# Kernel optimization log

Hardware: AMD Instinct MI355X
Metric: run time of the kernel (lower is better)

## Reference

```python
import jax, jax.numpy as jnp
import numpy as np
from jax import lax

# Config (matches init_kwargs)
B, CIN, H, W = 32, 256, 56, 56
COUT, KS, STRIDE, PAD, GROUPS = 256, 3, 1, 1, 2
CG_IN = CIN // GROUPS            # 128
OUT_F = COUT // GROUPS           # 128 per-group out features
IN_F = CG_IN * KS * KS           # 1152 per-group in features
Q = (IN_F * OUT_F // 4) * GROUPS # 73728 quadruplets total
TAU = 1.0

# All six 2-of-4 masking patterns (as in the torch module)
_MASK_PATTERNS = np.array([[0.,0.,1.,1.],[0.,1.,0.,1.],[0.,1.,1.,0.],
                           [1.,0.,0.,1.],[1.,0.,1.,0.],[1.,1.,0.,0.]], dtype=np.float32)


def setup_inputs() -> dict:
    key = jax.random.key(0)
    k1, k2, k3, k4 = jax.random.split(key, 4)
    x = jax.random.normal(k1, (B, CIN, H, W), dtype=jnp.float32)
    # per-group weight blocks, xavier-ish scale
    Ws = jax.random.normal(k2, (GROUPS, OUT_F, IN_F), dtype=jnp.float32) * 0.03
    choice_weights = jax.random.normal(k3, (Q, 6), dtype=jnp.float32)
    # gumbel noise: -log(Exp(1)) ~ Gumbel(0,1), matching -empty.exponential_().log()
    gumbels = -jnp.log(jax.random.exponential(k4, (Q, 6), dtype=jnp.float32))
    masking_patterns = jnp.asarray(_MASK_PATTERNS)
    return {"x": x, "Ws": Ws, "choice_weights": choice_weights,
            "gumbels": gumbels, "masking_patterns": masking_patterns}


def _hard_gumbel_softmax(logits, gumbels, tau):
    # straight-through hard gumbel softmax over last dim
    y_soft = jax.nn.softmax((logits + gumbels) / tau, axis=-1)
    idx = jnp.argmax(y_soft, axis=-1)
    y_hard = jax.nn.one_hot(idx, logits.shape[-1], dtype=logits.dtype)
    return y_hard - lax.stop_gradient(y_soft) + y_soft


def reference(x, Ws, choice_weights, gumbels, masking_patterns):
    # 1) sample 2:4 mask per quadruplet via hard gumbel-softmax choice over 6 patterns
    choice = _hard_gumbel_softmax(choice_weights, gumbels, TAU)   # (Q, 6)
    mask = choice @ masking_patterns                              # (Q, 4)
    mask = mask.reshape(GROUPS, OUT_F, IN_F)                      # quadruplets tile W row-major
    Wm = Ws * mask                                                # (G, OUT_F, IN_F)

    # 2) im2col (torch Unfold ordering: channel-major, then kh, kw)
    patches = lax.conv_general_dilated_patches(
        x, filter_shape=(KS, KS), window_strides=(STRIDE, STRIDE),
        padding=[(PAD, PAD), (PAD, PAD)])                         # (B, CIN*KS*KS, Ho, Wo)
    Ho = (H + 2 * PAD - KS) // STRIDE + 1
    Wo = (W + 2 * PAD - KS) // STRIDE + 1
    L = Ho * Wo
    # channel-major ordering => group g occupies contiguous IN_F rows
    patches = patches.reshape(B, GROUPS, IN_F, L)                 # (B, G, IN_F, L)

    # 3) per-group masked GEMM, no bias (use_bias=False)
    y = jnp.einsum('goi,bgil->bgol', Wm, patches)                 # (B, G, OUT_F, L)
    return y.reshape(B, COUT, Ho, Wo)
```

## Files before the change

### kernel.cpp

```cpp
#include <hip/hip_runtime.h>


#define INF   1152
#define HO    56
#define LOUT  3136
#define XP    58

typedef __attribute__((ext_vector_type(8))) short bf16x8;
typedef __attribute__((ext_vector_type(4))) float f32x4;

__device__ __forceinline__ unsigned short f2bf(float f) {
  union { float f; unsigned u; } v; v.f = f;
  unsigned r = v.u + 0x7fffu + ((v.u >> 16) & 1u);
  return (unsigned short)(r >> 16);
}

__device__ __forceinline__ void async_load16(const void* g, void* l) {
  __builtin_amdgcn_global_load_lds(
      (const __attribute__((address_space(1))) void*)g,
      (__attribute__((address_space(3))) void*)l, 16, 0, 0);
}

__global__ __launch_bounds__(256) void prep_kernel(
    const float* __restrict__ x, const float* __restrict__ Ws,
    const float* __restrict__ cw, const float* __restrict__ gb,
    const float* __restrict__ pat,
    unsigned short* __restrict__ Xt, unsigned short* __restrict__ Wt) {
  __shared__ float lds[56 * 129];
  const int t   = threadIdx.x;
  const int bid = blockIdx.x;

  if (bid >= 3712) {
    int idx = (bid - 3712) * 256 + t;
    int c   = idx & 127;
    int of  = (idx >> 7) & 127;
    int gt  = idx >> 14;
    int g   = gt / 9;
    int tap = gt - g * 9;
    int e   = ((g << 7) + of) * INF + c * 9 + tap;
    int q   = e >> 2, pos = e & 3;
    const float* cq = cw + q * 6;
    const float* gq = gb + q * 6;
    float best = cq[0] + gq[0]; int bi = 0;
    #pragma unroll
    for (int j = 1; j < 6; ++j) {
      float v2 = cq[j] + gq[j];
      if (v2 > best) { best = v2; bi = j; }
    }
    Wt[idx] = f2bf(Ws[e] * pat[bi * 4 + pos]);
    return;
  }

  const int bg  = bid / 58;
  const int ihp = bid - bg * 58;
  uint4* dst = (uint4*)(Xt + ((bg * XP + ihp) * XP) * 128);
  if (ihp == 0 || ihp == XP - 1) {
    const uint4 z = {0u, 0u, 0u, 0u};
    for (int i = t; i < XP * 16; i += 256) dst[i] = z;
    return;
  }
  const int ih = ihp - 1;
  const float4* src = (const float4*)(x + (bg * 128) * LOUT + ih * HO);
  for (int i = t; i < 128 * 14; i += 256) {
    int c = i / 14, seg = i - c * 14;
    float4 v = src[c * (LOUT / 4) + seg];
    float* row = &lds[(seg * 4) * 129 + c];
    row[0]       = v.x;
    row[129]     = v.y;
    row[2 * 129] = v.z;
    row[3 * 129] = v.w;
  }
  __syncthreads();
  for (int i = t; i < XP * 16; i += 256) {
    int iwp = i >> 4, oct = i & 15;
    uint4 val = {0u, 0u, 0u, 0u};
    if (iwp != 0 && iwp != XP - 1) {
      const float* s = &lds[(iwp - 1) * 129 + (oct << 3)];
      val.x = (unsigned)f2bf(s[0]) | ((unsigned)f2bf(s[1]) << 16);
      val.y = (unsigned)f2bf(s[2]) | ((unsigned)f2bf(s[3]) << 16);
      val.z = (unsigned)f2bf(s[4]) | ((unsigned)f2bf(s[5]) << 16);
      val.w = (unsigned)f2bf(s[6]) | ((unsigned)f2bf(s[7]) << 16);
    }
    dst[i] = val;
  }
}

__global__ __launch_bounds__(256, 4) void conv_mfma_kernel(
    const unsigned short* __restrict__ Wt, const unsigned short* __restrict__ Xt,
    float* __restrict__ out) {
  __shared__ __align__(16) unsigned short sA[128 * 64];
  __shared__ __align__(16) unsigned short sB[128 * 64];
  const int t  = threadIdx.x;
  const int ln = t & 63, wv = t >> 6;
  const int wm = wv >> 1, wn = wv & 1;
  const int col = ln & 15, kq = ln >> 4, c7 = col & 7;

  const int lid   = blockIdx.y * 25 + blockIdx.x;
  const int v     = (lid & 7) * 200 + (lid >> 3);
  const int bg    = v / 25;
  const int tileN = v - bg * 25;
  const int g     = bg & 1;
  const int l0    = tileN << 7;

  const int r8 = ln >> 3;
  const int ch = (ln & 7) ^ r8;
  int arow[4], brow[4];
  #pragma unroll
  for (int i = 0; i < 4; ++i) {
    const int rr = (wv << 5) + (i << 3) + r8;
    arow[i] = (rr << 7) + (ch << 3);
    int ll = l0 + rr;
    if (ll > LOUT - 1) ll = LOUT - 1;
    int oh = ll / HO, ow = ll - oh * HO;
    brow[i] = ((bg * XP + oh) * XP + ow) * 128 + (ch << 3);
  }

  f32x4 acc[4][4];
  #pragma unroll
  for (int i = 0; i < 4; ++i)
    #pragma unroll
    for (int j = 0; j < 4; ++j) acc[i][j] = (f32x4){0.f, 0.f, 0.f, 0.f};

  for (int tap = 0; tap < 9; ++tap) {
    const int th = tap / 3, tw = tap - th * 3;
    const int bTap = (th * XP + tw) << 7;
    const int aTap = (g * 9 + tap) << 14;
    #pragma unroll 1
    for (int kc = 0; kc < 2; ++kc) {
      const int c0 = kc << 6;
      __syncthreads();
      #pragma unroll
      for (int i = 0; i < 4; ++i) {
        const int lb = ((wv << 5) + (i << 3)) << 6;
        async_load16(Wt + aTap + c0 + arow[i], &sA[lb]);
        async_load16(Xt + bTap + c0 + brow[i], &sB[lb]);
      }
      __syncthreads();
      #pragma unroll
      for (int kh = 0; kh < 2; ++kh) {
        const int pk = (((kh << 2) + kq) ^ c7) << 3;
        bf16x8 af[4], bfr[4];
        #pragma unroll
        for (int mi = 0; mi < 4; ++mi)
          af[mi] = *(const bf16x8*)&sA[(((wm << 6) + (mi << 4) + col) << 6) + pk];
        #pragma unroll
        for (int ni = 0; ni < 4; ++ni)
          bfr[ni] = *(const bf16x8*)&sB[(((wn << 6) + (ni << 4) + col) << 6) + pk];
        #pragma unroll
        for (int mi = 0; mi < 4; ++mi)
          #pragma unroll
          for (int ni = 0; ni < 4; ++ni)
            acc[mi][ni] = __builtin_amdgcn_mfma_f32_16x16x32_bf16(
                af[mi], bfr[ni], acc[mi][ni], 0, 0, 0);
      }
    }
  }

  const int rowq = kq << 2;
  #pragma unroll
  for (int mi = 0; mi < 4; ++mi) {
    #pragma unroll
    for (int ni = 0; ni < 4; ++ni) {
      const int l = l0 + (wn << 6) + (ni << 4) + col;
      if (l < LOUT) {
        #pragma unroll
        for (int r = 0; r < 4; ++r) {
          const int of = (wm << 6) + (mi << 4) + rowq + r;
          out[(bg * 128 + of) * LOUT + l] = acc[mi][ni][r];
        }
      }
    }
  }
}

extern "C" void kernel_launch(void* const* d_in, const int* in_sizes, int n_in,
                              void* d_out, int out_size, void* d_ws, size_t ws_size,
                              hipStream_t stream) {
  const float* x   = (const float*)d_in[0];
  const float* Ws  = (const float*)d_in[1];
  const float* cw  = (const float*)d_in[2];
  const float* gb  = (const float*)d_in[3];
  const float* pat = (const float*)d_in[4];
  float* out = (float*)d_out;

  unsigned short* Wt = (unsigned short*)d_ws;
  unsigned short* Xt = (unsigned short*)((char*)d_ws + (1 << 20));

  prep_kernel<<<4864, 256, 0, stream>>>(x, Ws, cw, gb, pat, Xt, Wt);
  conv_mfma_kernel<<<dim3(25, 64), 256, 0, stream>>>(Wt, Xt, out);
}
```

Measured before the change: 254.4 us.

## Double-buffer LDS tiles to overlap async global loads with MFMA compute

Splits the A and B shared-memory tiles into two buffers and flattens the tap/channel-chunk loops into 18 stages. Each stage issues the async global-to-LDS loads for the next stage before running MFMAs on the current one, which removes one barrier per stage. LDS use doubles to 64 KB and the launch-bounds occupancy hint drops from 4 to 2 blocks per CU, so there may be fewer waves resident to hide latency.

```diff
diff --git a/kernel.cpp b/kernel.cpp
--- a/kernel.cpp
+++ b/kernel.cpp
@@ -85,11 +85,11 @@
   }
 }
 
-__global__ __launch_bounds__(256, 4) void conv_mfma_kernel(
+__global__ __launch_bounds__(256, 2) void conv_mfma_kernel(
     const unsigned short* __restrict__ Wt, const unsigned short* __restrict__ Xt,
     float* __restrict__ out) {
-  __shared__ __align__(16) unsigned short sA[128 * 64];
-  __shared__ __align__(16) unsigned short sB[128 * 64];
+  __shared__ __align__(16) unsigned short sA[2][128 * 64];
+  __shared__ __align__(16) unsigned short sB[2][128 * 64];
   const int t  = threadIdx.x;
   const int ln = t & 63, wv = t >> 6;
   const int wm = wv >> 1, wn = wv & 1;
@@ -121,39 +121,45 @@
     #pragma unroll
     for (int j = 0; j < 4; ++j) acc[i][j] = (f32x4){0.f, 0.f, 0.f, 0.f};
 
-  for (int tap = 0; tap < 9; ++tap) {
-    const int th = tap / 3, tw = tap - th * 3;
-    const int bTap = (th * XP + tw) << 7;
-    const int aTap = (g * 9 + tap) << 14;
-    #pragma unroll 1
-    for (int kc = 0; kc < 2; ++kc) {
-      const int c0 = kc << 6;
-      __syncthreads();
+  auto issue = [&](int s, int nxt) {
+    const int tap = s >> 1, kc = s & 1;
+    const int th  = (tap * 11) >> 5;
+    const int tw  = tap - th * 3;
+    const int bOff = ((th * XP + tw) << 7) + (kc << 6);
+    const int aOff = ((g * 9 + tap) << 14) + (kc << 6);
+    #pragma unroll
+    for (int i = 0; i < 4; ++i) {
+      const int lb = ((wv << 5) + (i << 3)) << 6;
+      async_load16(Wt + aOff + arow[i], &sA[nxt][lb]);
+      async_load16(Xt + bOff + brow[i], &sB[nxt][lb]);
+    }
+  };
+
+  issue(0, 0);
+  __syncthreads();
+
+  #pragma unroll 2
+  for (int s = 0; s < 18; ++s) {
+    const int cur = s & 1;
+    if (s < 17) issue(s + 1, cur ^ 1);
+    #pragma unroll
+    for (int kh = 0; kh < 2; ++kh) {
+      const int pk = (((kh << 2) + kq) ^ c7) << 3;
+      bf16x8 af[4], bfr[4];
       #pragma unroll
-      for (int i = 0; i < 4; ++i) {
-        const int lb = ((wv << 5) + (i << 3)) << 6;
-        async_load16(Wt + aTap + c0 + arow[i], &sA[lb]);
-        async_load16(Xt + bTap + c0 + brow[i], &sB[lb]);
-      }
-      __syncthreads();
+      for (int mi = 0; mi < 4; ++mi)
+        af[mi] = *(const bf16x8*)&sA[cur][(((wm << 6) + (mi << 4) + col) << 6) + pk];
       #pragma unroll
-      for (int kh = 0; kh < 2; ++kh) {
-        const int pk = (((kh << 2) + kq) ^ c7) << 3;
-        bf16x8 af[4], bfr[4];
-        #pragma unroll
-        for (int mi = 0; mi < 4; ++mi)
-          af[mi] = *(const bf16x8*)&sA[(((wm << 6) + (mi << 4) + col) << 6) + pk];
+      for (int ni = 0; ni < 4; ++ni)
+        bfr[ni] = *(const bf16x8*)&sB[cur][(((wn << 6) + (ni << 4) + col) << 6) + pk];
+      #pragma unroll
+      for (int mi = 0; mi < 4; ++mi)
         #pragma unroll
         for (int ni = 0; ni < 4; ++ni)
-          bfr[ni] = *(const bf16x8*)&sB[(((wn << 6) + (ni << 4) + col) << 6) + pk];
-        #pragma unroll
-        for (int mi = 0; mi < 4; ++mi)
-          #pragma unroll
-          for (int ni = 0; ni < 4; ++ni)
-            acc[mi][ni] = __builtin_amdgcn_mfma_f32_16x16x32_bf16(
-                af[mi], bfr[ni], acc[mi][ni], 0, 0, 0);
-      }
+          acc[mi][ni] = __builtin_amdgcn_mfma_f32_16x16x32_bf16(
+              af[mi], bfr[ni], acc[mi][ni], 0, 0, 0);
     }
+    __syncthreads();
   }
 
   const int rowq = kq << 2;
```

New measurement: 271.5 us. 6.7% more time.

## Stage input halo tile in LDS once per channel chunk and double-buffer weights

Applied to the files above, without the earlier changes.

Instead of reloading a fresh 128x64 im2col B tile for each of the 9 taps, each block loads a 6-row by 64-column padded input halo window (384 pixels x 64 channels) into LDS once per channel chunk. Each tap then reads its shifted window directly from that LDS tile, and the weight tile is double-buffered so the next tap's A load overlaps the current MFMAs. This cuts global/L2 traffic for the input by about 9x and removes one barrier per tap. In exchange LDS use rises to 80KB per block and the launch bound drops to 2 blocks per CU, lowering occupancy.

```diff
diff --git a/kernel.cpp b/kernel.cpp
--- a/kernel.cpp
+++ b/kernel.cpp
@@ -85,11 +85,11 @@
   }
 }
 
-__global__ __launch_bounds__(256, 4) void conv_mfma_kernel(
+__global__ __launch_bounds__(256, 2) void conv_mfma_kernel(
     const unsigned short* __restrict__ Wt, const unsigned short* __restrict__ Xt,
     float* __restrict__ out) {
-  __shared__ __align__(16) unsigned short sA[128 * 64];
-  __shared__ __align__(16) unsigned short sB[128 * 64];
+  __shared__ __align__(16) unsigned short sA[2][128 * 64];
+  __shared__ __align__(16) unsigned short sB[384 * 64];
   const int t  = threadIdx.x;
   const int ln = t & 63, wv = t >> 6;
   const int wm = wv >> 1, wn = wv & 1;
@@ -101,19 +101,32 @@
   const int tileN = v - bg * 25;
   const int g     = bg & 1;
   const int l0    = tileN << 7;
+  const int oh0   = l0 / HO;
 
   const int r8 = ln >> 3;
   const int ch = (ln & 7) ^ r8;
-  int arow[4], brow[4];
-  #pragma unroll
-  for (int i = 0; i < 4; ++i) {
-    const int rr = (wv << 5) + (i << 3) + r8;
-    arow[i] = (rr << 7) + (ch << 3);
-    int ll = l0 + rr;
-    if (ll > LOUT - 1) ll = LOUT - 1;
-    int oh = ll / HO, ow = ll - oh * HO;
-    brow[i] = ((bg * XP + oh) * XP + ow) * 128 + (ch << 3);
-  }
+  int arow[4];
+  #pragma unroll
+  for (int i = 0; i < 4; ++i)
+    arow[i] = (((wv << 5) + (i << 3) + r8) << 7) + (ch << 3);
+
+  const int p0    = t >> 3;
+  const int kB    = (t & 7) ^ (p0 & 7);
+  const int xbase = bg * (XP * XP * 128);
+
+  int pb[4];
+  #pragma unroll
+  for (int ni = 0; ni < 4; ++ni) {
+    int l = l0 + (wn << 6) + (ni << 4) + col;
+    if (l > LOUT - 1) l = LOUT - 1;
+    int oh = l / HO, ow = l - oh * HO;
+    pb[ni] = ((oh - oh0) << 6) + ow;
+  }
+
+  int aoffm[4];
+  #pragma unroll
+  for (int mi = 0; mi < 4; ++mi)
+    aoffm[mi] = (((wm << 6) + (mi << 4) + col) << 6) + ((kq ^ c7) << 3);
 
   f32x4 acc[4][4];
   #pragma unroll
@@ -121,31 +134,49 @@
     #pragma unroll
     for (int j = 0; j < 4; ++j) acc[i][j] = (f32x4){0.f, 0.f, 0.f, 0.f};
 
-  for (int tap = 0; tap < 9; ++tap) {
-    const int th = tap / 3, tw = tap - th * 3;
-    const int bTap = (th * XP + tw) << 7;
-    const int aTap = (g * 9 + tap) << 14;
-    #pragma unroll 1
-    for (int kc = 0; kc < 2; ++kc) {
-      const int c0 = kc << 6;
-      __syncthreads();
+  for (int kc = 0; kc < 2; ++kc) {
+    const int c0 = kc << 6;
+    #pragma unroll
+    for (int it = 0; it < 12; ++it) {
+      const int p   = (it << 5) + p0;
+      int ihp = oh0 + (p >> 6);  if (ihp > XP - 1) ihp = XP - 1;
+      int iwp = p & 63;          if (iwp > XP - 1) iwp = XP - 1;
+      async_load16(Xt + xbase + (ihp * XP + iwp) * 128 + c0 + (kB << 3),
+                   &sB[(it << 11) + (wv << 9)]);
+    }
+    #pragma unroll
+    for (int i = 0; i < 4; ++i)
+      async_load16(Wt + (g * 9 << 14) + c0 + arow[i],
+                   &sA[0][((wv << 5) + (i << 3)) << 6]);
+    __syncthreads();
+
+    for (int tap = 0; tap < 9; ++tap) {
+      const int cur = tap & 1;
+      if (tap < 8) {
+        const int aOff = ((g * 9 + tap + 1) << 14) + c0;
+        #pragma unroll
+        for (int i = 0; i < 4; ++i)
+          async_load16(Wt + aOff + arow[i],
+                       &sA[cur ^ 1][((wv << 5) + (i << 3)) << 6]);
+      }
+      const int th = (tap * 11) >> 5;
+      const int tw = tap - th * 3;
+      int boff[4];
       #pragma unroll
-      for (int i = 0; i < 4; ++i) {
-        const int lb = ((wv << 5) + (i << 3)) << 6;
-        async_load16(Wt + aTap + c0 + arow[i], &sA[lb]);
-        async_load16(Xt + bTap + c0 + brow[i], &sB[lb]);
-      }
-      __syncthreads();
+      for (int ni = 0; ni < 4; ++ni) {
+        const int p = pb[ni] + (th << 6) + tw;
+        boff[ni] = (p << 6) + ((kq ^ (p & 7)) << 3);
+      }
       #pragma unroll
       for (int kh = 0; kh < 2; ++kh) {
-        const int pk = (((kh << 2) + kq) ^ c7) << 3;
+        const int kx = kh << 5;
         bf16x8 af[4], bfr[4];
         #pragma unroll
         for (int mi = 0; mi < 4; ++mi)
-          af[mi] = *(const bf16x8*)&sA[(((wm << 6) + (mi << 4) + col) << 6) + pk];
+          af[mi] = *(const bf16x8*)&sA[cur][aoffm[mi] ^ kx];
         #pragma unroll
         for (int ni = 0; ni < 4; ++ni)
-          bfr[ni] = *(const bf16x8*)&sB[(((wn << 6) + (ni << 4) + col) << 6) + pk];
+          bfr[ni] = *(const bf16x8*)&sB[boff[ni] ^ kx];
         #pragma unroll
         for (int mi = 0; mi < 4; ++mi)
           #pragma unroll
@@ -153,6 +184,7 @@
             acc[mi][ni] = __builtin_amdgcn_mfma_f32_16x16x32_bf16(
                 af[mi], bfr[ni], acc[mi][ni], 0, 0, 0);
       }
+      __syncthreads();
     }
   }
 
```

After: 261.4 us. 1.03x slower.

## Stage input row-region once per channel chunk and reuse across all 9 taps

Applied to the files above, without the earlier changes.

Instead of reloading an im2col tile into LDS for each tap and channel half, the conv kernel stages a 6-row padded input region per 32-channel chunk into double-buffered LDS and reads all 9 tap-shifted fragments from it. The weight matrix is pre-permuted in prep into MFMA fragment order so A fragments load straight from global memory into registers, prefetched one step ahead, with no LDS staging. This cuts LDS fill traffic and barriers (two syncs per 64 channels become one per 32-channel chunk) and enables overlap, at the cost of more LDS per block and lower occupancy (launch bounds 4 to 3).

```diff
diff --git a/kernel.cpp b/kernel.cpp
--- a/kernel.cpp
+++ b/kernel.cpp
@@ -47,7 +47,10 @@
       float v2 = cq[j] + gq[j];
       if (v2 > best) { best = v2; bi = j; }
     }
-    Wt[idx] = f2bf(Ws[e] * pat[bi * 4 + pos]);
+    const int kc = c >> 5, kq = (c >> 3) & 3, e8 = c & 7;
+    const int ofb = of >> 4, colA = of & 15;
+    const int dst = ((gt * 4 + kc) * 32 + ofb * 4 + kq) * 128 + colA * 8 + e8;
+    Wt[dst] = f2bf(Ws[e] * pat[bi * 4 + pos]);
     return;
   }
 
@@ -85,15 +88,14 @@
   }
 }
 
-__global__ __launch_bounds__(256, 4) void conv_mfma_kernel(
+__global__ __launch_bounds__(256, 3) void conv_mfma_kernel(
     const unsigned short* __restrict__ Wt, const unsigned short* __restrict__ Xt,
     float* __restrict__ out) {
-  __shared__ __align__(16) unsigned short sA[128 * 64];
-  __shared__ __align__(16) unsigned short sB[128 * 64];
+  __shared__ __align__(16) unsigned short sB[2][6 * 64 * 32];
   const int t  = threadIdx.x;
   const int ln = t & 63, wv = t >> 6;
   const int wm = wv >> 1, wn = wv & 1;
-  const int col = ln & 15, kq = ln >> 4, c7 = col & 7;
+  const int col = ln & 15, kq = ln >> 4;
 
   const int lid   = blockIdx.y * 25 + blockIdx.x;
   const int v     = (lid & 7) * 200 + (lid >> 3);
@@ -101,19 +103,23 @@
   const int tileN = v - bg * 25;
   const int g     = bg & 1;
   const int l0    = tileN << 7;
-
-  const int r8 = ln >> 3;
-  const int ch = (ln & 7) ^ r8;
-  int arow[4], brow[4];
+  const int oh0   = l0 / HO;
+
+  const int iwp0 = t >> 2;
+  const int iwpc = iwp0 > XP - 1 ? XP - 1 : iwp0;
+  const int csrc = (t & 3) ^ ((iwp0 >> 1) & 3);
+  const int xbase = bg * (XP * XP * 128);
+
+  int pb[4];
   #pragma unroll
-  for (int i = 0; i < 4; ++i) {
-    const int rr = (wv << 5) + (i << 3) + r8;
-    arow[i] = (rr << 7) + (ch << 3);
-    int ll = l0 + rr;
-    if (ll > LOUT - 1) ll = LOUT - 1;
-    int oh = ll / HO, ow = ll - oh * HO;
-    brow[i] = ((bg * XP + oh) * XP + ow) * 128 + (ch << 3);
-  }
+  for (int ni = 0; ni < 4; ++ni) {
+    int l = l0 + (wn << 6) + (ni << 4) + col;
+    if (l > LOUT - 1) l = LOUT - 1;
+    int oh = l / HO, ow = l - oh * HO;
+    pb[ni] = ((oh - oh0) << 6) + ow;
+  }
+
+  const unsigned short* aptr = Wt + (g * 9 * 4) * 4096 + wm * 2048 + ln * 8;
 
   f32x4 acc[4][4];
   #pragma unroll
@@ -121,39 +127,56 @@
     #pragma unroll
     for (int j = 0; j < 4; ++j) acc[i][j] = (f32x4){0.f, 0.f, 0.f, 0.f};
 
-  for (int tap = 0; tap < 9; ++tap) {
-    const int th = tap / 3, tw = tap - th * 3;
-    const int bTap = (th * XP + tw) << 7;
-    const int aTap = (g * 9 + tap) << 14;
-    #pragma unroll 1
-    for (int kc = 0; kc < 2; ++kc) {
-      const int c0 = kc << 6;
-      __syncthreads();
+  auto stageRegion = [&](int kcR, int buf) {
+    const int c0 = kcR << 5;
+    #pragma unroll
+    for (int it = 0; it < 6; ++it) {
+      int ihp = oh0 + it; if (ihp > XP - 1) ihp = XP - 1;
+      async_load16(Xt + xbase + (ihp * XP + iwpc) * 128 + c0 + (csrc << 3),
+                   &sB[buf][it * 2048 + t * 8]);
+    }
+  };
+
+  auto loadA = [&](int kcL, int tapL, bf16x8* dst) {
+    const unsigned short* p = aptr + (tapL * 4 + kcL) * 4096;
+    #pragma unroll
+    for (int mi = 0; mi < 4; ++mi) dst[mi] = *(const bf16x8*)(p + mi * 512);
+  };
+
+  bf16x8 afA[4], afB[4];
+  stageRegion(0, 0);
+  loadA(0, 0, afA);
+  __syncthreads();
+
+  #pragma unroll 1
+  for (int kc = 0; kc < 4; ++kc) {
+    const int cur = kc & 1;
+    #pragma unroll
+    for (int tap = 0; tap < 9; ++tap) {
+      const bool last = (kc == 3 && tap == 8);
+      if (!last)
+        loadA(tap == 8 ? kc + 1 : kc, tap == 8 ? 0 : tap + 1, afB);
+      if (tap == 1 && kc < 3) stageRegion(kc + 1, cur ^ 1);
+      const int th = tap / 3, tw = tap - th * 3;
+      bf16x8 bfr[4];
       #pragma unroll
-      for (int i = 0; i < 4; ++i) {
-        const int lb = ((wv << 5) + (i << 3)) << 6;
-        async_load16(Wt + aTap + c0 + arow[i], &sA[lb]);
-        async_load16(Xt + bTap + c0 + brow[i], &sB[lb]);
+      for (int ni = 0; ni < 4; ++ni) {
+        const int pos = pb[ni] + (th << 6) + tw;
+        bfr[ni] = *(const bf16x8*)
+            &sB[cur][pos * 32 + ((kq ^ ((pos >> 1) & 3)) << 3)];
       }
-      __syncthreads();
       #pragma unroll
-      for (int kh = 0; kh < 2; ++kh) {
-        const int pk = (((kh << 2) + kq) ^ c7) << 3;
-        bf16x8 af[4], bfr[4];
-        #pragma unroll
-        for (int mi = 0; mi < 4; ++mi)
-          af[mi] = *(const bf16x8*)&sA[(((wm << 6) + (mi << 4) + col) << 6) + pk];
+      for (int mi = 0; mi < 4; ++mi)
         #pragma unroll
         for (int ni = 0; ni < 4; ++ni)
-          bfr[ni] = *(const bf16x8*)&sB[(((wn << 6) + (ni << 4) + col) << 6) + pk];
+          acc[mi][ni] = __builtin_amdgcn_mfma_f32_16x16x32_bf16(
+              afA[mi], bfr[ni], acc[mi][ni], 0, 0, 0);
+      if (!last) {
         #pragma unroll
-        for (int mi = 0; mi < 4; ++mi)
-          #pragma unroll
-          for (int ni = 0; ni < 4; ++ni)
-            acc[mi][ni] = __builtin_amdgcn_mfma_f32_16x16x32_bf16(
-                af[mi], bfr[ni], acc[mi][ni], 0, 0, 0);
+        for (int mi = 0; mi < 4; ++mi) afA[mi] = afB[mi];
       }
     }
+    __syncthreads();
   }
 
   const int rowq = kq << 2;
```

Measured after the change: 319.6 us. +25.6%, slower.
